# Kernel tuning notes

Measured on AMD Instinct MI355X. Metric: run time of the kernel, lower is better.

The kernel has to match this reference:

```python
import jax, jax.numpy as jnp
import numpy as np

EVENTLEN = 8  # config.event_length
NEG = -10000.0


def setup_inputs() -> dict:
    key = jax.random.key(0)
    k1, k2 = jax.random.split(key)
    T, B, E = 128, 512, 128  # decodelen, batch_size, entity_size
    feats = jax.random.normal(k1, (T, B, E), dtype=jnp.float32)
    transitions = jax.random.normal(k2, (E, E), dtype=jnp.float32)
    # Same masking the torch module applies to transitions.data at init
    transitions = transitions.at[0, :].set(NEG).at[:, -1].set(NEG)
    return {"feats": feats, "transitions": transitions}


def reference(feats, transitions):
    """Segmented CRF forward algorithm (OneCrfCCKSDecoder._forward_alg).

    feats:       [T, B, E] per-step emission scores (entity tag logits)
    transitions: [E, E]    transitions[j, k] = score of k -> j
    Returns scalar alpha / (T // EVENTLEN).
    """
    T, B, E = feats.shape
    n_events = T // EVENTLEN

    # Faithful to torch: init_alphas[:][0] = 0.0 zeroes the batch-0 ROW.
    init_fv = jnp.full((B, E), NEG, dtype=feats.dtype).at[0].set(0.0)

    t_idx = jnp.arange(T)
    is_boundary = (t_idx % EVENTLEN == 0) & (t_idx != 0)  # accumulate alpha
    is_update = (t_idx % EVENTLEN != 0)                   # DP update step

    def step(carry, inp):
        fv, alpha = carry              # fv: [B, E], alpha: scalar
        feat, bnd, upd = inp           # feat: [B, E]
        # Event-boundary accumulation (uses fv BEFORE any update; note the
        # original never resets fv inside _forward_alg).
        alpha_inc = jnp.mean(jax.nn.logsumexp(fv + transitions[-1], axis=1))
        alpha = alpha + jnp.where(bnd, alpha_inc, jnp.zeros_like(alpha_inc))
        # fv_new[b, j] = logsumexp_k( fv[b,k] + feat[b,k] + transitions[j,k] )
        x = fv + feat                                        # [B, E]
        fv_new = jax.nn.logsumexp(x[:, None, :] + transitions[None, :, :], axis=-1)
        fv = jnp.where(upd, fv_new, fv)
        return (fv, alpha), None

    (fv, alpha), _ = jax.lax.scan(
        step, (init_fv, jnp.zeros((), feats.dtype)), (feats, is_boundary, is_update)
    )
    # Terminal accumulation after the loop.
    alpha = alpha + jnp.mean(jax.nn.logsumexp(fv + transitions[-1], axis=1))
    return alpha / n_events
```

## Files before the change

kernel.cpp:

```cpp
#include <hip/hip_runtime.h>


typedef _Float16 f16x4 __attribute__((ext_vector_type(4)));
typedef _Float16 f16x8 __attribute__((ext_vector_type(8)));
typedef float    f32x4 __attribute__((ext_vector_type(4)));

#define NEG_VAL   (-10000.0f)
#define C_SCALE   0.0024787521766663585f
#define LOG_C     6.0f

#define LDS_BARRIER() asm volatile("s_waitcnt lgkmcnt(0)\n\ts_barrier" ::: "memory")

__global__ __launch_bounds__(256)
void prep_exp(const float* __restrict__ feats, _Float16* __restrict__ ef)
{
    int id = blockIdx.x * 256 + threadIdx.x;
    #pragma unroll
    for (int it = 0; it < 4; ++it, id += 524288) {
        const int jj = id & 31;
        const int tb = id >> 5;
        const int b  = tb & 511;
        const int t  = tb >> 9;
        f32x4 x = *(const f32x4*)(feats + (size_t)tb * 128 + 4 * jj);
        auto lo = __builtin_amdgcn_cvt_pkrtz(__expf(x[0]) * C_SCALE,
                                             __expf(x[1]) * C_SCALE);
        auto hi = __builtin_amdgcn_cvt_pkrtz(__expf(x[2]) * C_SCALE,
                                             __expf(x[3]) * C_SCALE);
        f16x4 o;
        o[0] = (_Float16)lo[0]; o[1] = (_Float16)lo[1];
        o[2] = (_Float16)hi[0]; o[3] = (_Float16)hi[1];
        const int off = t * 65536 + (b >> 4) * 2048 + (jj >> 2) * 256
                      + (b & 15) * 16 + (jj & 3) * 4;
        *(f16x4*)(ef + off) = o;
    }
}

__device__ inline f16x4 cvt4(f32x4 a) {
    auto lo = __builtin_amdgcn_cvt_pkrtz(a[0], a[1]);
    auto hi = __builtin_amdgcn_cvt_pkrtz(a[2], a[3]);
    f16x4 o;
    o[0] = (_Float16)lo[0]; o[1] = (_Float16)lo[1];
    o[2] = (_Float16)hi[0]; o[3] = (_Float16)hi[1];
    return o;
}

__global__ __launch_bounds__(512)
void crf_fwd(const _Float16* __restrict__ ef,
             const float* __restrict__ trans,
             float* __restrict__ out)
{
    const int tid  = threadIdx.x;
    const int w    = tid >> 6;
    const int lane = tid & 63;
    const int bloc = lane & 15;
    const int q    = lane >> 4;
    const int b    = blockIdx.x * 16 + bloc;

    f16x8 Afrag[4];
    {
        const float* rowp = trans + (size_t)(16 * w + bloc) * 128;
        #pragma unroll
        for (int kap = 0; kap < 4; ++kap) {
            const f32x4* p = (const f32x4*)(rowp + 32 * kap + 8 * q);
            f32x4 x = p[0], y = p[1];
            f16x8 f;
            f[0] = (_Float16)__expf(x[0]); f[1] = (_Float16)__expf(x[1]);
            f[2] = (_Float16)__expf(x[2]); f[3] = (_Float16)__expf(x[3]);
            f[4] = (_Float16)__expf(y[0]); f[5] = (_Float16)__expf(y[1]);
            f[6] = (_Float16)__expf(y[2]); f[7] = (_Float16)__expf(y[3]);
            Afrag[kap] = f;
        }
    }
    f32x4 te;
    {
        f32x4 x = *(const f32x4*)(trans + 127 * 128 + 16 * w + 4 * q);
        te[0] = __expf(x[0]); te[1] = __expf(x[1]);
        te[2] = __expf(x[2]); te[3] = __expf(x[3]);
    }

    __shared__ __align__(16) char  Hbuf[8192];
    __shared__ float Spart[16 * 8];
    __shared__ float Mpart[16 * 8];

    const int waddr = bloc * 256 + (((2 * w + (q >> 1)) ^ bloc) * 16) + 8 * (q & 1);
    int raddr[4];
    #pragma unroll
    for (int kap = 0; kap < 4; ++kap)
        raddr[kap] = bloc * 256 + (((4 * kap + q) ^ bloc) * 16);

    const _Float16* efb = ef + blockIdx.x * 2048 + w * 256 + bloc * 16 + q * 4;
    f16x4 cur, nx1, nx2;
    cur = *(const f16x4*)(efb + 1 * 65536);
    nx1 = *(const f16x4*)(efb + 2 * 65536);
    nx2 = *(const f16x4*)(efb + 3 * 65536);

    f32x4 acc = {1.f, 1.f, 1.f, 1.f};
    float M     = (b == 0) ? 0.0f : NEG_VAL;
    float alpha = 0.0f;
    int hb = 0;

    #pragma unroll 8
    for (int t = 1; t < 128; ++t) {
        const bool upd = (t & 7) != 0;

        if (upd) {
            M += LOG_C;
            f16x4 hh = cvt4(acc) * cur;
            *(f16x4*)(Hbuf + hb + waddr) = hh;
            LDS_BARRIER();

            f16x8 B0 = *(const f16x8*)(Hbuf + hb + raddr[0]);
            f16x8 B1 = *(const f16x8*)(Hbuf + hb + raddr[1]);
            f16x8 B2 = *(const f16x8*)(Hbuf + hb + raddr[2]);
            f16x8 B3 = *(const f16x8*)(Hbuf + hb + raddr[3]);

            f32x4 z = {0.f, 0.f, 0.f, 0.f};
            f32x4 da = __builtin_amdgcn_mfma_f32_16x16x32_f16(Afrag[0], B0, z, 0, 0, 0);
            f32x4 db = __builtin_amdgcn_mfma_f32_16x16x32_f16(Afrag[1], B1, z, 0, 0, 0);
            da = __builtin_amdgcn_mfma_f32_16x16x32_f16(Afrag[2], B2, da, 0, 0, 0);
            db = __builtin_amdgcn_mfma_f32_16x16x32_f16(Afrag[3], B3, db, 0, 0, 0);
            acc = da + db;
            hb ^= 4096;
        } else {
            float s = acc[0] * te[0] + acc[1] * te[1]
                    + acc[2] * te[2] + acc[3] * te[3];
            float m = fmaxf(fmaxf(acc[0], acc[1]), fmaxf(acc[2], acc[3]));
            s += __shfl_xor(s, 16, 64);
            s += __shfl_xor(s, 32, 64);
            m = fmaxf(m, __shfl_xor(m, 16, 64));
            m = fmaxf(m, __shfl_xor(m, 32, 64));
            if (q == 0) {
                Spart[bloc * 8 + w] = s;
                Mpart[bloc * 8 + w] = m;
            }
            LDS_BARRIER();

            f32x4 sa = *(const f32x4*)&Spart[bloc * 8];
            f32x4 sb = *(const f32x4*)&Spart[bloc * 8 + 4];
            f32x4 ma = *(const f32x4*)&Mpart[bloc * 8];
            f32x4 mb = *(const f32x4*)&Mpart[bloc * 8 + 4];
            float r = ((sa[0] + sa[1]) + (sa[2] + sa[3]))
                    + ((sb[0] + sb[1]) + (sb[2] + sb[3]));
            float cmax = fmaxf(fmaxf(fmaxf(ma[0], ma[1]), fmaxf(ma[2], ma[3])),
                               fmaxf(fmaxf(mb[0], mb[1]), fmaxf(mb[2], mb[3])));

            alpha += M + __logf(r);
            const float inv = __builtin_amdgcn_rcpf(cmax);
            acc[0] *= inv; acc[1] *= inv; acc[2] *= inv; acc[3] *= inv;
            M += __logf(cmax);
        }

        if (t + 1 < 128) {
            cur = nx1;
            nx1 = nx2;
            if (t + 3 < 128) nx2 = *(const f16x4*)(efb + (size_t)(t + 3) * 65536);
        }
    }

    {
        float s = acc[0] * te[0] + acc[1] * te[1]
                + acc[2] * te[2] + acc[3] * te[3];
        s += __shfl_xor(s, 16, 64);
        s += __shfl_xor(s, 32, 64);
        if (q == 0) Spart[bloc * 8 + w] = s;
        LDS_BARRIER();
        f32x4 sa = *(const f32x4*)&Spart[bloc * 8];
        f32x4 sb = *(const f32x4*)&Spart[bloc * 8 + 4];
        float r = ((sa[0] + sa[1]) + (sa[2] + sa[3]))
                + ((sb[0] + sb[1]) + (sb[2] + sb[3]));
        alpha += M + __logf(r);
    }

    if (w == 0) {
        float v = alpha;
        #pragma unroll
        for (int off = 1; off < 64; off <<= 1)
            v += __shfl_xor(v, off, 64);
        if (lane == 0)
            atomicAdd(out, v * (1.0f / (4.0f * 512.0f * 16.0f)));
    }
}

extern "C" void kernel_launch(void* const* d_in, const int* in_sizes, int n_in,
                              void* d_out, int out_size, void* d_ws, size_t ws_size,
                              hipStream_t stream) {
    const float* feats = (const float*)d_in[0];
    const float* trans = (const float*)d_in[1];
    float* out = (float*)d_out;
    _Float16* ef = (_Float16*)d_ws;

    (void)hipMemsetAsync(out, 0, sizeof(float), stream);
    prep_exp<<<2048, 256, 0, stream>>>(feats, ef);
    crf_fwd<<<32, 512, 0, stream>>>(ef, trans, out);
}
```

Measured before the change: 106.2 us.

## Fuse exp prep into CRF kernel with producer warps feeding an LDS ring

Removes the separate prep_exp kernel and its f16 workspace round trip. The CRF kernel is launched with 1024 threads: 8 consumer waves run the MFMA recurrence, and 8 producer waves load fp32 feats, exponentiate and scale them, and write f16 values into a 4-slot LDS ring two steps ahead. This hides the exp and global-load cost behind the serial recurrence and saves one kernel launch. In exchange every step now hits a barrier across all 16 waves, and producer and consumer waves compete for issue slots on the same CU.

```diff
diff --git a/kernel.cpp b/kernel.cpp
--- a/kernel.cpp
+++ b/kernel.cpp
@@ -11,30 +11,6 @@
 
 #define LDS_BARRIER() asm volatile("s_waitcnt lgkmcnt(0)\n\ts_barrier" ::: "memory")
 
-__global__ __launch_bounds__(256)
-void prep_exp(const float* __restrict__ feats, _Float16* __restrict__ ef)
-{
-    int id = blockIdx.x * 256 + threadIdx.x;
-    #pragma unroll
-    for (int it = 0; it < 4; ++it, id += 524288) {
-        const int jj = id & 31;
-        const int tb = id >> 5;
-        const int b  = tb & 511;
-        const int t  = tb >> 9;
-        f32x4 x = *(const f32x4*)(feats + (size_t)tb * 128 + 4 * jj);
-        auto lo = __builtin_amdgcn_cvt_pkrtz(__expf(x[0]) * C_SCALE,
-                                             __expf(x[1]) * C_SCALE);
-        auto hi = __builtin_amdgcn_cvt_pkrtz(__expf(x[2]) * C_SCALE,
-                                             __expf(x[3]) * C_SCALE);
-        f16x4 o;
-        o[0] = (_Float16)lo[0]; o[1] = (_Float16)lo[1];
-        o[2] = (_Float16)hi[0]; o[3] = (_Float16)hi[1];
-        const int off = t * 65536 + (b >> 4) * 2048 + (jj >> 2) * 256
-                      + (b & 15) * 16 + (jj & 3) * 4;
-        *(f16x4*)(ef + off) = o;
-    }
-}
-
 __device__ inline f16x4 cvt4(f32x4 a) {
     auto lo = __builtin_amdgcn_cvt_pkrtz(a[0], a[1]);
     auto hi = __builtin_amdgcn_cvt_pkrtz(a[2], a[3]);
@@ -44,8 +20,15 @@
     return o;
 }
 
-__global__ __launch_bounds__(512)
-void crf_fwd(const _Float16* __restrict__ ef,
+__device__ inline f16x4 expC4(f32x4 x) {
+    f32x4 e;
+    e[0] = __expf(x[0]) * C_SCALE; e[1] = __expf(x[1]) * C_SCALE;
+    e[2] = __expf(x[2]) * C_SCALE; e[3] = __expf(x[3]) * C_SCALE;
+    return cvt4(e);
+}
+
+__global__ __launch_bounds__(1024, 1)
+void crf_fwd(const float* __restrict__ feats,
              const float* __restrict__ trans,
              float* __restrict__ out)
 {
@@ -55,9 +38,29 @@
     const int bloc = lane & 15;
     const int q    = lane >> 4;
     const int b    = blockIdx.x * 16 + bloc;
+    const bool prod = (w >= 8);
+
+    __shared__ __align__(16) char      Hbuf[8192];
+    __shared__ __align__(16) _Float16  EFring[4][2048];
+    __shared__ float Spart[128];
+    __shared__ float Mpart[128];
 
     f16x8 Afrag[4];
-    {
+    f32x4 te;
+    const int waddr = bloc * 256 + (((2 * w + (q >> 1)) ^ bloc) * 16) + 8 * (q & 1);
+    int raddr[4];
+    #pragma unroll
+    for (int kap = 0; kap < 4; ++kap)
+        raddr[kap] = bloc * 256 + (((4 * kap + q) ^ bloc) * 16);
+    const int eoff = w * 256 + bloc * 16 + q * 4;
+    f16x4 cur;
+
+    const int pw   = w - 8;
+    const int poff = pw * 256 + bloc * 16 + q * 4;
+    const float* fptr = feats + (size_t)b * 128 + 16 * pw + 4 * q;
+    f32x4 rA, rB;
+
+    if (!prod) {
         const float* rowp = trans + (size_t)(16 * w + bloc) * 128;
         #pragma unroll
         for (int kap = 0; kap < 4; ++kap) {
@@ -70,29 +73,19 @@
             f[6] = (_Float16)__expf(y[2]); f[7] = (_Float16)__expf(y[3]);
             Afrag[kap] = f;
         }
-    }
-    f32x4 te;
-    {
         f32x4 x = *(const f32x4*)(trans + 127 * 128 + 16 * w + 4 * q);
         te[0] = __expf(x[0]); te[1] = __expf(x[1]);
         te[2] = __expf(x[2]); te[3] = __expf(x[3]);
+    } else {
+        f32x4 x1 = *(const f32x4*)(fptr + 1 * 65536);
+        f32x4 x2 = *(const f32x4*)(fptr + 2 * 65536);
+        *(f16x4*)&EFring[1][poff] = expC4(x1);
+        *(f16x4*)&EFring[2][poff] = expC4(x2);
+        rA = *(const f32x4*)(fptr + 3 * 65536);
+        rB = *(const f32x4*)(fptr + 4 * 65536);
     }
-
-    __shared__ __align__(16) char  Hbuf[8192];
-    __shared__ float Spart[16 * 8];
-    __shared__ float Mpart[16 * 8];
-
-    const int waddr = bloc * 256 + (((2 * w + (q >> 1)) ^ bloc) * 16) + 8 * (q & 1);
-    int raddr[4];
-    #pragma unroll
-    for (int kap = 0; kap < 4; ++kap)
-        raddr[kap] = bloc * 256 + (((4 * kap + q) ^ bloc) * 16);
-
-    const _Float16* efb = ef + blockIdx.x * 2048 + w * 256 + bloc * 16 + q * 4;
-    f16x4 cur, nx1, nx2;
-    cur = *(const f16x4*)(efb + 1 * 65536);
-    nx1 = *(const f16x4*)(efb + 2 * 65536);
-    nx2 = *(const f16x4*)(efb + 3 * 65536);
+    LDS_BARRIER();
+    if (!prod) cur = *(const f16x4*)&EFring[1][eoff];
 
     f32x4 acc = {1.f, 1.f, 1.f, 1.f};
     float M     = (b == 0) ? 0.0f : NEG_VAL;
@@ -103,81 +96,89 @@
     for (int t = 1; t < 128; ++t) {
         const bool upd = (t & 7) != 0;
 
-        if (upd) {
-            M += LOG_C;
-            f16x4 hh = cvt4(acc) * cur;
-            *(f16x4*)(Hbuf + hb + waddr) = hh;
-            LDS_BARRIER();
-
-            f16x8 B0 = *(const f16x8*)(Hbuf + hb + raddr[0]);
-            f16x8 B1 = *(const f16x8*)(Hbuf + hb + raddr[1]);
-            f16x8 B2 = *(const f16x8*)(Hbuf + hb + raddr[2]);
-            f16x8 B3 = *(const f16x8*)(Hbuf + hb + raddr[3]);
-
-            f32x4 z = {0.f, 0.f, 0.f, 0.f};
-            f32x4 da = __builtin_amdgcn_mfma_f32_16x16x32_f16(Afrag[0], B0, z, 0, 0, 0);
-            f32x4 db = __builtin_amdgcn_mfma_f32_16x16x32_f16(Afrag[1], B1, z, 0, 0, 0);
-            da = __builtin_amdgcn_mfma_f32_16x16x32_f16(Afrag[2], B2, da, 0, 0, 0);
-            db = __builtin_amdgcn_mfma_f32_16x16x32_f16(Afrag[3], B3, db, 0, 0, 0);
-            acc = da + db;
-            hb ^= 4096;
+        if (!prod) {
+            if (upd) {
+                M += LOG_C;
+                f16x4 hh = cvt4(acc) * cur;
+                *(f16x4*)(Hbuf + hb + waddr) = hh;
+            } else {
+                float s = acc[0] * te[0] + acc[1] * te[1]
+                        + acc[2] * te[2] + acc[3] * te[3];
+                float m = fmaxf(fmaxf(acc[0], acc[1]), fmaxf(acc[2], acc[3]));
+                s += __shfl_xor(s, 16, 64);
+                s += __shfl_xor(s, 32, 64);
+                m = fmaxf(m, __shfl_xor(m, 16, 64));
+                m = fmaxf(m, __shfl_xor(m, 32, 64));
+                if (q == 0) {
+                    Spart[bloc * 8 + w] = s;
+                    Mpart[bloc * 8 + w] = m;
+                }
+            }
         } else {
-            float s = acc[0] * te[0] + acc[1] * te[1]
-                    + acc[2] * te[2] + acc[3] * te[3];
-            float m = fmaxf(fmaxf(acc[0], acc[1]), fmaxf(acc[2], acc[3]));
-            s += __shfl_xor(s, 16, 64);
-            s += __shfl_xor(s, 32, 64);
-            m = fmaxf(m, __shfl_xor(m, 16, 64));
-            m = fmaxf(m, __shfl_xor(m, 32, 64));
-            if (q == 0) {
-                Spart[bloc * 8 + w] = s;
-                Mpart[bloc * 8 + w] = m;
-            }
-            LDS_BARRIER();
-
-            f32x4 sa = *(const f32x4*)&Spart[bloc * 8];
-            f32x4 sb = *(const f32x4*)&Spart[bloc * 8 + 4];
-            f32x4 ma = *(const f32x4*)&Mpart[bloc * 8];
-            f32x4 mb = *(const f32x4*)&Mpart[bloc * 8 + 4];
-            float r = ((sa[0] + sa[1]) + (sa[2] + sa[3]))
-                    + ((sb[0] + sb[1]) + (sb[2] + sb[3]));
-            float cmax = fmaxf(fmaxf(fmaxf(ma[0], ma[1]), fmaxf(ma[2], ma[3])),
-                               fmaxf(fmaxf(mb[0], mb[1]), fmaxf(mb[2], mb[3])));
-
-            alpha += M + __logf(r);
-            const float inv = __builtin_amdgcn_rcpf(cmax);
-            acc[0] *= inv; acc[1] *= inv; acc[2] *= inv; acc[3] *= inv;
-            M += __logf(cmax);
+            const int tn = t + 2;
+            if (tn <= 127 && (tn & 7) != 0)
+                *(f16x4*)&EFring[tn & 3][poff] = expC4(rA);
+            rA = rB;
+            if (t + 4 <= 127) rB = *(const f32x4*)(fptr + (size_t)(t + 4) * 65536);
         }
 
-        if (t + 1 < 128) {
-            cur = nx1;
-            nx1 = nx2;
-            if (t + 3 < 128) nx2 = *(const f16x4*)(efb + (size_t)(t + 3) * 65536);
+        LDS_BARRIER();
+
+        if (!prod) {
+            if (upd) {
+                f16x8 B0 = *(const f16x8*)(Hbuf + hb + raddr[0]);
+                f16x8 B1 = *(const f16x8*)(Hbuf + hb + raddr[1]);
+                f16x8 B2 = *(const f16x8*)(Hbuf + hb + raddr[2]);
+                f16x8 B3 = *(const f16x8*)(Hbuf + hb + raddr[3]);
+                f32x4 z = {0.f, 0.f, 0.f, 0.f};
+                f32x4 da = __builtin_amdgcn_mfma_f32_16x16x32_f16(Afrag[0], B0, z, 0, 0, 0);
+                f32x4 db = __builtin_amdgcn_mfma_f32_16x16x32_f16(Afrag[1], B1, z, 0, 0, 0);
+                da = __builtin_amdgcn_mfma_f32_16x16x32_f16(Afrag[2], B2, da, 0, 0, 0);
+                db = __builtin_amdgcn_mfma_f32_16x16x32_f16(Afrag[3], B3, db, 0, 0, 0);
+                acc = da + db;
+                hb ^= 4096;
+            } else {
+                f32x4 sa = *(const f32x4*)&Spart[bloc * 8];
+                f32x4 sb = *(const f32x4*)&Spart[bloc * 8 + 4];
+                f32x4 ma = *(const f32x4*)&Mpart[bloc * 8];
+                f32x4 mb = *(const f32x4*)&Mpart[bloc * 8 + 4];
+                float r = ((sa[0] + sa[1]) + (sa[2] + sa[3]))
+                        + ((sb[0] + sb[1]) + (sb[2] + sb[3]));
+                float cmax = fmaxf(fmaxf(fmaxf(ma[0], ma[1]), fmaxf(ma[2], ma[3])),
+                                   fmaxf(fmaxf(mb[0], mb[1]), fmaxf(mb[2], mb[3])));
+                alpha += M + __logf(r);
+                const float inv = __builtin_amdgcn_rcpf(cmax);
+                acc[0] *= inv; acc[1] *= inv; acc[2] *= inv; acc[3] *= inv;
+                M += __logf(cmax);
+            }
+            if (t + 1 < 128 && ((t + 1) & 7) != 0)
+                cur = *(const f16x4*)&EFring[(t + 1) & 3][eoff];
         }
     }
 
-    {
+    if (!prod) {
         float s = acc[0] * te[0] + acc[1] * te[1]
                 + acc[2] * te[2] + acc[3] * te[3];
         s += __shfl_xor(s, 16, 64);
         s += __shfl_xor(s, 32, 64);
         if (q == 0) Spart[bloc * 8 + w] = s;
-        LDS_BARRIER();
+    }
+    LDS_BARRIER();
+    if (!prod) {
         f32x4 sa = *(const f32x4*)&Spart[bloc * 8];
         f32x4 sb = *(const f32x4*)&Spart[bloc * 8 + 4];
         float r = ((sa[0] + sa[1]) + (sa[2] + sa[3]))
                 + ((sb[0] + sb[1]) + (sb[2] + sb[3]));
         alpha += M + __logf(r);
-    }
 
-    if (w == 0) {
-        float v = alpha;
-        #pragma unroll
-        for (int off = 1; off < 64; off <<= 1)
-            v += __shfl_xor(v, off, 64);
-        if (lane == 0)
-            atomicAdd(out, v * (1.0f / (4.0f * 512.0f * 16.0f)));
+        if (w == 0) {
+            float v = alpha;
+            #pragma unroll
+            for (int off = 1; off < 64; off <<= 1)
+                v += __shfl_xor(v, off, 64);
+            if (lane == 0)
+                atomicAdd(out, v * (1.0f / (4.0f * 512.0f * 16.0f)));
+        }
     }
 }
 
@@ -187,9 +188,7 @@
     const float* feats = (const float*)d_in[0];
     const float* trans = (const float*)d_in[1];
     float* out = (float*)d_out;
-    _Float16* ef = (_Float16*)d_ws;
 
     (void)hipMemsetAsync(out, 0, sizeof(float), stream);
-    prep_exp<<<2048, 256, 0, stream>>>(feats, ef);
-    crf_fwd<<<32, 512, 0, stream>>>(ef, trans, out);
+    crf_fwd<<<32, 1024, 0, stream>>>(feats, trans, out);
 }
```

After: 128.7 us. 21.1% more time.

## Fuse emission exp/fp16 conversion into the CRF recurrence kernel

Applied to the files above, without the earlier changes.

Removes the separate prep kernel that exponentiated feats into an fp16 workspace. The recurrence kernel now loads raw fp32 feats two steps ahead and computes exp, scale and fp16 conversion inline, one step before use. This saves a kernel launch and a full read-then-write pass over the emissions. In exchange the serial recurrence does extra exp work per step and loads twice as many bytes of fp32 on its latency-critical path, all from only 32 blocks.

```diff
diff --git a/kernel.cpp b/kernel.cpp
--- a/kernel.cpp
+++ b/kernel.cpp
@@ -11,30 +11,6 @@
 
 #define LDS_BARRIER() asm volatile("s_waitcnt lgkmcnt(0)\n\ts_barrier" ::: "memory")
 
-__global__ __launch_bounds__(256)
-void prep_exp(const float* __restrict__ feats, _Float16* __restrict__ ef)
-{
-    int id = blockIdx.x * 256 + threadIdx.x;
-    #pragma unroll
-    for (int it = 0; it < 4; ++it, id += 524288) {
-        const int jj = id & 31;
-        const int tb = id >> 5;
-        const int b  = tb & 511;
-        const int t  = tb >> 9;
-        f32x4 x = *(const f32x4*)(feats + (size_t)tb * 128 + 4 * jj);
-        auto lo = __builtin_amdgcn_cvt_pkrtz(__expf(x[0]) * C_SCALE,
-                                             __expf(x[1]) * C_SCALE);
-        auto hi = __builtin_amdgcn_cvt_pkrtz(__expf(x[2]) * C_SCALE,
-                                             __expf(x[3]) * C_SCALE);
-        f16x4 o;
-        o[0] = (_Float16)lo[0]; o[1] = (_Float16)lo[1];
-        o[2] = (_Float16)hi[0]; o[3] = (_Float16)hi[1];
-        const int off = t * 65536 + (b >> 4) * 2048 + (jj >> 2) * 256
-                      + (b & 15) * 16 + (jj & 3) * 4;
-        *(f16x4*)(ef + off) = o;
-    }
-}
-
 __device__ inline f16x4 cvt4(f32x4 a) {
     auto lo = __builtin_amdgcn_cvt_pkrtz(a[0], a[1]);
     auto hi = __builtin_amdgcn_cvt_pkrtz(a[2], a[3]);
@@ -44,8 +20,15 @@
     return o;
 }
 
+__device__ inline f16x4 expC4(f32x4 x) {
+    f32x4 e;
+    e[0] = __expf(x[0]) * C_SCALE; e[1] = __expf(x[1]) * C_SCALE;
+    e[2] = __expf(x[2]) * C_SCALE; e[3] = __expf(x[3]) * C_SCALE;
+    return cvt4(e);
+}
+
 __global__ __launch_bounds__(512)
-void crf_fwd(const _Float16* __restrict__ ef,
+void crf_fwd(const float* __restrict__ feats,
              const float* __restrict__ trans,
              float* __restrict__ out)
 {
@@ -88,11 +71,13 @@
     for (int kap = 0; kap < 4; ++kap)
         raddr[kap] = bloc * 256 + (((4 * kap + q) ^ bloc) * 16);
 
-    const _Float16* efb = ef + blockIdx.x * 2048 + w * 256 + bloc * 16 + q * 4;
-    f16x4 cur, nx1, nx2;
-    cur = *(const f16x4*)(efb + 1 * 65536);
-    nx1 = *(const f16x4*)(efb + 2 * 65536);
-    nx2 = *(const f16x4*)(efb + 3 * 65536);
+    const float* fb = feats + (size_t)b * 128 + 16 * w + 4 * q;
+    f16x4 cur, nxt;
+    f32x4 r2v, r3v;
+    cur = expC4(*(const f32x4*)(fb + 1 * 65536));
+    nxt = expC4(*(const f32x4*)(fb + 2 * 65536));
+    r2v = *(const f32x4*)(fb + 3 * 65536);
+    r3v = *(const f32x4*)(fb + 4 * 65536);
 
     f32x4 acc = {1.f, 1.f, 1.f, 1.f};
     float M     = (b == 0) ? 0.0f : NEG_VAL;
@@ -151,9 +136,10 @@
         }
 
         if (t + 1 < 128) {
-            cur = nx1;
-            nx1 = nx2;
-            if (t + 3 < 128) nx2 = *(const f16x4*)(efb + (size_t)(t + 3) * 65536);
+            cur = nxt;
+            if (t + 2 < 128) nxt = expC4(r2v);
+            r2v = r3v;
+            if (t + 4 < 128) r3v = *(const f32x4*)(fb + (size_t)(t + 4) * 65536);
         }
     }
 
@@ -187,9 +173,7 @@
     const float* feats = (const float*)d_in[0];
     const float* trans = (const float*)d_in[1];
     float* out = (float*)d_out;
-    _Float16* ef = (_Float16*)d_ws;
 
     (void)hipMemsetAsync(out, 0, sizeof(float), stream);
-    prep_exp<<<2048, 256, 0, stream>>>(feats, ef);
-    crf_fwd<<<32, 512, 0, stream>>>(ef, trans, out);
+    crf_fwd<<<32, 512, 0, stream>>>(feats, trans, out);
 }
```

Measured after the change: 155.7 us. 1.47x slower.
